# Performance work log

Measured on AMD Instinct MI355X. Metric: run time of the kernel, lower is better.

Reference implementation:

```python
import jax, jax.numpy as jnp
import numpy as np

N_NODES = 100_000
DEG = 16
N_EDGES = N_NODES * DEG
NODE_F = 128
EDGE_F = 16
HID = 64
B = 64
K = DEG


def setup_inputs() -> dict:
    key = jax.random.key(0)
    ks = jax.random.split(key, 12)
    # node i's outgoing edges are at ids i + k*N_NODES for k in [0, DEG)
    src = jnp.arange(N_EDGES, dtype=jnp.int32) % N_NODES
    dst = jax.random.randint(ks[0], (N_EDGES,), 0, N_NODES, dtype=jnp.int32)
    edge_index = jnp.stack([src, dst])
    current_nodes = jax.random.randint(ks[1], (B,), 0, N_NODES, dtype=jnp.int32)
    # reachable neighbors = destinations of the current node's real edges
    neighbor_nodes = dst[current_nodes[:, None] + jnp.arange(K, dtype=jnp.int32)[None, :] * N_NODES]
    x = jax.random.normal(ks[2], (N_NODES, NODE_F), jnp.float32)
    edge_attr = jax.random.normal(ks[3], (N_EDGES, EDGE_F), jnp.float32)
    return dict(
        x=x,
        edge_attr=edge_attr,
        conv1_W=jax.random.normal(ks[4], (NODE_F, HID), jnp.float32) * (NODE_F ** -0.5),
        conv1_b=jnp.zeros((HID,), jnp.float32),
        conv2_W=jax.random.normal(ks[5], (HID, HID), jnp.float32) * (HID ** -0.5),
        conv2_b=jnp.zeros((HID,), jnp.float32),
        mlp_W1=jax.random.normal(ks[6], (2 * HID + EDGE_F, 2 * HID), jnp.float32) * ((2 * HID + EDGE_F) ** -0.5),
        mlp_b1=jnp.zeros((2 * HID,), jnp.float32),
        mlp_W2=jax.random.normal(ks[7], (2 * HID, 1), jnp.float32) * ((2 * HID) ** -0.5),
        mlp_b2=jnp.zeros((1,), jnp.float32),
        edge_index=edge_index,
        current_nodes=current_nodes,
        neighbor_nodes=neighbor_nodes,
    )


def gcn_conv(x, edge_index, W, b):
    """PyG GCNConv: symmetric norm with self-loops, then linear + bias."""
    n = x.shape[0]
    loop = jnp.arange(n, dtype=edge_index.dtype)
    src = jnp.concatenate([edge_index[0], loop])  # messages flow src -> dst
    dst = jnp.concatenate([edge_index[1], loop])
    xw = x @ W                                    # [N, H]
    deg = jnp.zeros((n,), xw.dtype).at[dst].add(1.0)
    dinv = jnp.where(deg > 0, jax.lax.rsqrt(deg), 0.0)
    msg = (dinv[src] * dinv[dst])[:, None] * xw[src]      # [E+N, H]
    return jax.ops.segment_sum(msg, dst, num_segments=n) + b


def reference(x, edge_attr, conv1_W, conv1_b, conv2_W, conv2_b,
              mlp_W1, mlp_b1, mlp_W2, mlp_b2,
              edge_index, current_nodes, neighbor_nodes):
    n = x.shape[0]
    h = jax.nn.relu(gcn_conv(x, edge_index, conv1_W, conv1_b))
    h = jax.nn.relu(gcn_conv(h, edge_index, conv2_W, conv2_b))

    # First edge id matching each (current, neighbor) pair, replacing the
    # original O(E)-per-neighbor boolean-mask loop with a sorted-key lookup.
    keys = edge_index[0].astype(jnp.int64) * n + edge_index[1].astype(jnp.int64)
    order = jnp.argsort(keys, stable=True)        # stable -> leftmost == first edge id
    skeys = keys[order]
    query = current_nodes[:, None].astype(jnp.int64) * n + neighbor_nodes.astype(jnp.int64)
    pos = jnp.clip(jnp.searchsorted(skeys, query), 0, skeys.shape[0] - 1)
    valid = skeys[pos] == query                   # [B, K]
    eid = order[pos]
    ea = edge_attr[eid]                           # [B, K, F]

    b_, k_ = neighbor_nodes.shape
    h_cur = jnp.broadcast_to(h[current_nodes][:, None, :], (b_, k_, h.shape[1]))
    h_nbr = h[neighbor_nodes]
    m = jnp.concatenate([h_cur, h_nbr, ea], axis=-1)  # [B, K, 2H+F]
    q = (jax.nn.relu(m @ mlp_W1 + mlp_b1) @ mlp_W2 + mlp_b2)[..., 0]
    q = jnp.where(valid, q, 0.0)
    return q, valid
```

## Files before the change

kernel.cpp:

```cpp
#include <hip/hip_runtime.h>

#define N_NODES 100000
#define DEG 16
#define N_EDGES (N_NODES * DEG)
#define NODE_F 128
#define EDGE_F 16
#define HID 64
#define NQ 1024
#define NCHUNK (N_EDGES / 256)
#define XTILES ((N_NODES + 63) / 64)
#define NHIST 2048
#define BCAP 56
#define NDINV ((N_NODES + 255) / 256)
#define MAGIC 0x13579BDF

__device__ __forceinline__ int xcc_id() {
  int x;
  asm("s_getreg_b32 %0, hwreg(HW_REG_XCC_ID)" : "=s"(x));
  return x & 7;
}

__global__ void k_query_zero(const int* __restrict__ dst, const int* __restrict__ cur,
                             const int* __restrict__ nbr, int* __restrict__ n1,
                             int* __restrict__ n2, int* __restrict__ wcur,
                             int* __restrict__ eid_sel, float* __restrict__ out_valid,
                             int* __restrict__ degp) {
  if (blockIdx.x >= 4) {
    int4* d4 = (int4*)degp;
    const int n4 = 8 * N_NODES / 4;
    int i = (blockIdx.x - 4) * 256 + threadIdx.x;
    const int stride = (gridDim.x - 4) * 256;
    for (; i < n4; i += stride) d4[i] = make_int4(0, 0, 0, 0);
    return;
  }
  int i = blockIdx.x * 256 + threadIdx.x;
  if (i >= NQ) return;
  int b = i >> 4;
  int c = cur[b];
  int nb = nbr[i];
  int sel = -1;
  #pragma unroll
  for (int j = 0; j < DEG; ++j) {
    int e = c + j * N_NODES;
    if (sel < 0 && dst[e] == nb) sel = e;
  }
  eid_sel[i] = sel;
  out_valid[i] = (sel >= 0) ? 1.0f : 0.0f;
  n2[c] = MAGIC; n2[nb] = MAGIC;
  n1[c] = MAGIC; n1[nb] = MAGIC;
  wcur[c] = 0;   wcur[nb] = 0;
}

__global__ __launch_bounds__(256) void k_fusedA(
    const float* __restrict__ x, const float* __restrict__ Wg,
    float* __restrict__ xw, const int* __restrict__ dst,
    const int* __restrict__ n2, int* __restrict__ n1, int* __restrict__ wcur,
    int* __restrict__ degp) {
  __shared__ float xs[64 * 128];
  const int t = threadIdx.x;

  if (blockIdx.x < NHIST) {
    int* __restrict__ dp = degp + (size_t)xcc_id() * N_NODES;
    const int stride = NHIST * 256;
    for (int e = blockIdx.x * 256 + t; e < N_EDGES; e += stride) {
      int d = dst[e];
      __hip_atomic_fetch_add(&dp[d], 1, __ATOMIC_RELAXED,
                             __HIP_MEMORY_SCOPE_WORKGROUP);
      if (n2[d] == MAGIC) {
        int s = e % N_NODES;
        n1[s] = MAGIC;
        wcur[s] = 0;
      }
    }
    return;
  }

  const int lane = t & 63;
  const int w = __builtin_amdgcn_readfirstlane(t >> 6);
  const long base = (long)(blockIdx.x - NHIST) * 64;

  const float4* __restrict__ xv = (const float4*)x;
  #pragma unroll
  for (int p = 0; p < 8; ++p) {
    int f4 = p * 256 + t;
    int r = f4 >> 5;
    int c4 = f4 & 31;
    long gr = base + r;
    float4 v = (gr < N_NODES) ? xv[gr * 32 + c4]
                              : make_float4(0.f, 0.f, 0.f, 0.f);
    int rs = r & 31;
    float* xr = xs + r * 128;
    xr[((c4 << 2) + 0) ^ rs] = v.x;
    xr[((c4 << 2) + 1) ^ rs] = v.y;
    xr[((c4 << 2) + 2) ^ rs] = v.z;
    xr[((c4 << 2) + 3) ^ rs] = v.w;
  }
  __syncthreads();

  float acc[16];
  #pragma unroll
  for (int j = 0; j < 16; ++j) acc[j] = 0.f;
  const int ls = lane & 31;
  const float* __restrict__ xrow = xs + lane * 128;
  const float4* __restrict__ wp = (const float4*)(Wg + w * 16);
  #pragma unroll 4
  for (int k = 0; k < NODE_F; ++k) {
    float xk = xrow[k ^ ls];
    float4 w0 = wp[k * 16 + 0];
    float4 w1 = wp[k * 16 + 1];
    float4 w2 = wp[k * 16 + 2];
    float4 w3 = wp[k * 16 + 3];
    acc[ 0] = fmaf(xk, w0.x, acc[ 0]); acc[ 1] = fmaf(xk, w0.y, acc[ 1]);
    acc[ 2] = fmaf(xk, w0.z, acc[ 2]); acc[ 3] = fmaf(xk, w0.w, acc[ 3]);
    acc[ 4] = fmaf(xk, w1.x, acc[ 4]); acc[ 5] = fmaf(xk, w1.y, acc[ 5]);
    acc[ 6] = fmaf(xk, w1.z, acc[ 6]); acc[ 7] = fmaf(xk, w1.w, acc[ 7]);
    acc[ 8] = fmaf(xk, w2.x, acc[ 8]); acc[ 9] = fmaf(xk, w2.y, acc[ 9]);
    acc[10] = fmaf(xk, w2.z, acc[10]); acc[11] = fmaf(xk, w2.w, acc[11]);
    acc[12] = fmaf(xk, w3.x, acc[12]); acc[13] = fmaf(xk, w3.y, acc[13]);
    acc[14] = fmaf(xk, w3.z, acc[14]); acc[15] = fmaf(xk, w3.w, acc[15]);
  }
  long gr = base + lane;
  if (gr < N_NODES) {
    float4* __restrict__ op = (float4*)(xw + gr * HID + w * 16);
    op[0] = make_float4(acc[0], acc[1], acc[2], acc[3]);
    op[1] = make_float4(acc[4], acc[5], acc[6], acc[7]);
    op[2] = make_float4(acc[8], acc[9], acc[10], acc[11]);
    op[3] = make_float4(acc[12], acc[13], acc[14], acc[15]);
  }
}

__global__ void k_bucket_dinv(const int* __restrict__ dst, const int* __restrict__ n1,
                              int* __restrict__ wcur, int* __restrict__ bucket,
                              const int* __restrict__ degp, float* __restrict__ dinv) {
  if (blockIdx.x < NDINV) {
    int v = blockIdx.x * 256 + threadIdx.x;
    if (v < N_NODES) {
      int s = 1;
      #pragma unroll
      for (int p = 0; p < 8; ++p) s += degp[(size_t)p * N_NODES + v];
      dinv[v] = rsqrtf((float)s);
    }
    return;
  }
  int e = (blockIdx.x - NDINV) * 256 + threadIdx.x;
  int d = dst[e];
  if (n1[d] != MAGIC) return;
  int pos = atomicAdd(&wcur[d], 1);
  if (pos >= 0 && pos < BCAP)
    bucket[(size_t)d * BCAP + pos] = e % N_NODES;
}

__global__ __launch_bounds__(256) void k_gather_xw2(
    const int* __restrict__ bucket, const int* __restrict__ wcur,
    const int* __restrict__ n1, const float* __restrict__ dinv,
    const float* __restrict__ xw, const float* __restrict__ bias,
    const float* __restrict__ W2g, float* __restrict__ xw2) {
  const int t = threadIdx.x;
  const int lane = t & 63;
  const int v = blockIdx.x * 4 + (t >> 6);
  if (v >= N_NODES) return;
  if (n1[v] != MAGIC) return;
  int n = wcur[v];
  if (n > BCAP) n = BCAP;
  if (n < 0) n = 0;
  int   s_l = (lane < n) ? bucket[(size_t)v * BCAP + lane] : 0;
  float w_l = (lane < n) ? dinv[s_l] : 0.f;
  float acc = 0.f;
  int j = 0;
  for (; j + 3 < n; j += 4) {
    int s0 = __shfl(s_l, j);
    int s1 = __shfl(s_l, j + 1);
    int s2 = __shfl(s_l, j + 2);
    int s3 = __shfl(s_l, j + 3);
    float a0 = xw[(size_t)s0 * HID + lane];
    float a1 = xw[(size_t)s1 * HID + lane];
    float a2 = xw[(size_t)s2 * HID + lane];
    float a3 = xw[(size_t)s3 * HID + lane];
    acc = fmaf(__shfl(w_l, j), a0, acc);
    acc = fmaf(__shfl(w_l, j + 1), a1, acc);
    acc = fmaf(__shfl(w_l, j + 2), a2, acc);
    acc = fmaf(__shfl(w_l, j + 3), a3, acc);
  }
  for (; j < n; ++j)
    acc = fmaf(__shfl(w_l, j), xw[(size_t)__shfl(s_l, j) * HID + lane], acc);
  float dv = dinv[v];
  acc = fmaf(dv, xw[(size_t)v * HID + lane], acc);
  float h = fmaxf(fmaf(dv, acc, bias[lane]), 0.f);
  float a2s = 0.f;
  #pragma unroll
  for (int f = 0; f < HID; ++f)
    a2s = fmaf(__shfl(h, f), W2g[f * HID + lane], a2s);
  xw2[(size_t)v * HID + lane] = a2s;
}

__global__ __launch_bounds__(256) void k_gather(
    const int* __restrict__ bucket, const int* __restrict__ wcur,
    const int* __restrict__ flag, const float* __restrict__ dinv,
    const float* __restrict__ xw, const float* __restrict__ bias,
    float* __restrict__ hout) {
  const int t = threadIdx.x;
  const int lane = t & 63;
  const int v = blockIdx.x * 4 + (t >> 6);
  if (v >= N_NODES) return;
  if (flag[v] != MAGIC) return;
  int n = wcur[v];
  if (n > BCAP) n = BCAP;
  if (n < 0) n = 0;
  int   s_l = (lane < n) ? bucket[(size_t)v * BCAP + lane] : 0;
  float w_l = (lane < n) ? dinv[s_l] : 0.f;
  float acc = 0.f;
  int j = 0;
  for (; j + 3 < n; j += 4) {
    int s0 = __shfl(s_l, j);
    int s1 = __shfl(s_l, j + 1);
    int s2 = __shfl(s_l, j + 2);
    int s3 = __shfl(s_l, j + 3);
    float a0 = xw[(size_t)s0 * HID + lane];
    float a1 = xw[(size_t)s1 * HID + lane];
    float a2 = xw[(size_t)s2 * HID + lane];
    float a3 = xw[(size_t)s3 * HID + lane];
    acc = fmaf(__shfl(w_l, j), a0, acc);
    acc = fmaf(__shfl(w_l, j + 1), a1, acc);
    acc = fmaf(__shfl(w_l, j + 2), a2, acc);
    acc = fmaf(__shfl(w_l, j + 3), a3, acc);
  }
  for (; j < n; ++j)
    acc = fmaf(__shfl(w_l, j), xw[(size_t)__shfl(s_l, j) * HID + lane], acc);
  float dv = dinv[v];
  acc = fmaf(dv, xw[(size_t)v * HID + lane], acc);
  hout[(size_t)v * HID + lane] = fmaxf(fmaf(dv, acc, bias[lane]), 0.f);
}

__global__ void k_mlp(const float* __restrict__ h2, const float* __restrict__ ea,
                      const float* __restrict__ W1, const float* __restrict__ b1,
                      const float* __restrict__ W2, const float* __restrict__ b2,
                      const int* __restrict__ cur, const int* __restrict__ nbr,
                      const int* __restrict__ eid_sel, float* __restrict__ out) {
  __shared__ float m[2 * HID + EDGE_F];
  __shared__ float red[128];
  const int q = blockIdx.x;
  const int t = threadIdx.x;
  const int eid = eid_sel[q];
  if (eid < 0) {
    if (t == 0) out[q] = 0.0f;
    return;
  }
  const int b = q >> 4;
  const int c = cur[b];
  const int nb = nbr[q];
  if (t < HID)    m[t] = h2[(size_t)c * HID + t];
  else            m[t] = h2[(size_t)nb * HID + (t - HID)];
  if (t < EDGE_F) m[2 * HID + t] = ea[(size_t)eid * EDGE_F + t];
  __syncthreads();
  float h = b1[t];
  #pragma unroll
  for (int j = 0; j < 2 * HID + EDGE_F; ++j) h = fmaf(m[j], W1[j * 128 + t], h);
  h = fmaxf(h, 0.f) * W2[t];
  red[t] = h;
  __syncthreads();
  if (t < 64) {
    float v = red[t] + red[t + 64];
    #pragma unroll
    for (int o = 32; o > 0; o >>= 1) v += __shfl_down(v, o);
    if (t == 0) out[q] = v + b2[0];
  }
}

extern "C" void kernel_launch(void* const* d_in, const int* in_sizes, int n_in,
                              void* d_out, int out_size, void* d_ws, size_t ws_size,
                              hipStream_t stream) {
  const float* x    = (const float*)d_in[0];
  const float* ea   = (const float*)d_in[1];
  const float* c1W  = (const float*)d_in[2];
  const float* c1b  = (const float*)d_in[3];
  const float* c2W  = (const float*)d_in[4];
  const float* c2b  = (const float*)d_in[5];
  const float* mW1  = (const float*)d_in[6];
  const float* mb1  = (const float*)d_in[7];
  const float* mW2  = (const float*)d_in[8];
  const float* mb2  = (const float*)d_in[9];
  const int*   eidx = (const int*)d_in[10];
  const int*   cur  = (const int*)d_in[11];
  const int*   nbr  = (const int*)d_in[12];
  const int* edst = eidx + N_EDGES;
  float* out = (float*)d_out;

  char* p = (char*)d_ws;
  auto alloc = [&](size_t bytes) -> void* {
    void* r = (void*)p;
    p += (bytes + 255) & ~(size_t)255;
    return r;
  };
  int*   degp    = (int*)alloc((size_t)8 * N_NODES * 4);
  float* dinv    = (float*)alloc((size_t)N_NODES * 4);
  int*   n1      = (int*)alloc((size_t)N_NODES * 4);
  int*   n2      = (int*)alloc((size_t)N_NODES * 4);
  int*   wcur    = (int*)alloc((size_t)N_NODES * 4);
  int*   eid_sel = (int*)alloc((size_t)NQ * 4);
  int*   bucket  = (int*)alloc((size_t)N_NODES * BCAP * 4);
  float* xw1     = (float*)alloc((size_t)N_NODES * HID * 4);
  float* xw2     = (float*)alloc((size_t)N_NODES * HID * 4);
  float* h2      = xw1;

  k_query_zero<<<260, 256, 0, stream>>>(edst, cur, nbr, n1, n2, wcur, eid_sel,
                                        out + NQ, degp);
  k_fusedA<<<NHIST + XTILES, 256, 0, stream>>>(x, c1W, xw1, edst, n2, n1, wcur,
                                               degp);
  k_bucket_dinv<<<NDINV + NCHUNK, 256, 0, stream>>>(edst, n1, wcur, bucket, degp,
                                                    dinv);
  k_gather_xw2<<<(N_NODES + 3) / 4, 256, 0, stream>>>(bucket, wcur, n1, dinv, xw1,
                                                      c1b, c2W, xw2);
  k_gather<<<(N_NODES + 3) / 4, 256, 0, stream>>>(bucket, wcur, n2, dinv, xw2,
                                                  c2b, h2);
  k_mlp<<<NQ, 128, 0, stream>>>(h2, ea, mW1, mb1, mW2, mb2, cur, nbr, eid_sel, out);
}
```

Before: 356.0 us.

## Interleave histogram blocks among smaller 32-row GEMM tiles in fused kernel

```diff
diff --git a/kernel.cpp b/kernel.cpp
--- a/kernel.cpp
+++ b/kernel.cpp
@@ -8,8 +8,9 @@
 #define HID 64
 #define NQ 1024
 #define NCHUNK (N_EDGES / 256)
-#define XTILES ((N_NODES + 63) / 64)
 #define NHIST 2048
+#define XT32 (N_NODES / 32)
+#define TOTAL_A (NHIST + XT32)
 #define BCAP 56
 #define NDINV ((N_NODES + 255) / 256)
 #define MAGIC 0x13579BDF
@@ -56,13 +57,17 @@
     float* __restrict__ xw, const int* __restrict__ dst,
     const int* __restrict__ n2, int* __restrict__ n1, int* __restrict__ wcur,
     int* __restrict__ degp) {
-  __shared__ float xs[64 * 128];
+  __shared__ float xs[32 * 128];
   const int t = threadIdx.x;
-
-  if (blockIdx.x < NHIST) {
+  const int bid = blockIdx.x;
+
+  const int h0 = (int)(((long)bid * NHIST) / TOTAL_A);
+  const int h1b = (int)(((long)(bid + 1) * NHIST) / TOTAL_A);
+
+  if (h1b > h0) {
     int* __restrict__ dp = degp + (size_t)xcc_id() * N_NODES;
     const int stride = NHIST * 256;
-    for (int e = blockIdx.x * 256 + t; e < N_EDGES; e += stride) {
+    for (int e = h0 * 256 + t; e < N_EDGES; e += stride) {
       int d = dst[e];
       __hip_atomic_fetch_add(&dp[d], 1, __ATOMIC_RELAXED,
                              __HIP_MEMORY_SCOPE_WORKGROUP);
@@ -75,58 +80,44 @@
     return;
   }
 
-  const int lane = t & 63;
-  const int w = __builtin_amdgcn_readfirstlane(t >> 6);
-  const long base = (long)(blockIdx.x - NHIST) * 64;
+  const long base = (long)(bid - h0) * 32;
 
   const float4* __restrict__ xv = (const float4*)x;
   #pragma unroll
-  for (int p = 0; p < 8; ++p) {
+  for (int p = 0; p < 4; ++p) {
     int f4 = p * 256 + t;
     int r = f4 >> 5;
     int c4 = f4 & 31;
-    long gr = base + r;
-    float4 v = (gr < N_NODES) ? xv[gr * 32 + c4]
-                              : make_float4(0.f, 0.f, 0.f, 0.f);
-    int rs = r & 31;
+    float4 v = xv[(base + r) * 32 + c4];
     float* xr = xs + r * 128;
-    xr[((c4 << 2) + 0) ^ rs] = v.x;
-    xr[((c4 << 2) + 1) ^ rs] = v.y;
-    xr[((c4 << 2) + 2) ^ rs] = v.z;
-    xr[((c4 << 2) + 3) ^ rs] = v.w;
+    xr[((c4 << 2) + 0) ^ r] = v.x;
+    xr[((c4 << 2) + 1) ^ r] = v.y;
+    xr[((c4 << 2) + 2) ^ r] = v.z;
+    xr[((c4 << 2) + 3) ^ r] = v.w;
   }
   __syncthreads();
 
-  float acc[16];
-  #pragma unroll
-  for (int j = 0; j < 16; ++j) acc[j] = 0.f;
-  const int ls = lane & 31;
-  const float* __restrict__ xrow = xs + lane * 128;
-  const float4* __restrict__ wp = (const float4*)(Wg + w * 16);
+  float acc[8];
+  #pragma unroll
+  for (int j = 0; j < 8; ++j) acc[j] = 0.f;
+  const int r = t & 31;
+  const int cg = t >> 5;
+  const float* __restrict__ xrow = xs + r * 128;
+  const float4* __restrict__ wp = (const float4*)(Wg + cg * 8);
   #pragma unroll 4
   for (int k = 0; k < NODE_F; ++k) {
-    float xk = xrow[k ^ ls];
+    float xk = xrow[k ^ r];
     float4 w0 = wp[k * 16 + 0];
     float4 w1 = wp[k * 16 + 1];
-    float4 w2 = wp[k * 16 + 2];
-    float4 w3 = wp[k * 16 + 3];
-    acc[ 0] = fmaf(xk, w0.x, acc[ 0]); acc[ 1] = fmaf(xk, w0.y, acc[ 1]);
-    acc[ 2] = fmaf(xk, w0.z, acc[ 2]); acc[ 3] = fmaf(xk, w0.w, acc[ 3]);
-    acc[ 4] = fmaf(xk, w1.x, acc[ 4]); acc[ 5] = fmaf(xk, w1.y, acc[ 5]);
-    acc[ 6] = fmaf(xk, w1.z, acc[ 6]); acc[ 7] = fmaf(xk, w1.w, acc[ 7]);
-    acc[ 8] = fmaf(xk, w2.x, acc[ 8]); acc[ 9] = fmaf(xk, w2.y, acc[ 9]);
-    acc[10] = fmaf(xk, w2.z, acc[10]); acc[11] = fmaf(xk, w2.w, acc[11]);
-    acc[12] = fmaf(xk, w3.x, acc[12]); acc[13] = fmaf(xk, w3.y, acc[13]);
-    acc[14] = fmaf(xk, w3.z, acc[14]); acc[15] = fmaf(xk, w3.w, acc[15]);
-  }
-  long gr = base + lane;
-  if (gr < N_NODES) {
-    float4* __restrict__ op = (float4*)(xw + gr * HID + w * 16);
-    op[0] = make_float4(acc[0], acc[1], acc[2], acc[3]);
-    op[1] = make_float4(acc[4], acc[5], acc[6], acc[7]);
-    op[2] = make_float4(acc[8], acc[9], acc[10], acc[11]);
-    op[3] = make_float4(acc[12], acc[13], acc[14], acc[15]);
-  }
+    acc[0] = fmaf(xk, w0.x, acc[0]); acc[1] = fmaf(xk, w0.y, acc[1]);
+    acc[2] = fmaf(xk, w0.z, acc[2]); acc[3] = fmaf(xk, w0.w, acc[3]);
+    acc[4] = fmaf(xk, w1.x, acc[4]); acc[5] = fmaf(xk, w1.y, acc[5]);
+    acc[6] = fmaf(xk, w1.z, acc[6]); acc[7] = fmaf(xk, w1.w, acc[7]);
+  }
+  long gr = base + r;
+  float4* __restrict__ op = (float4*)(xw + gr * HID + cg * 8);
+  op[0] = make_float4(acc[0], acc[1], acc[2], acc[3]);
+  op[1] = make_float4(acc[4], acc[5], acc[6], acc[7]);
 }
 
 __global__ void k_bucket_dinv(const int* __restrict__ dst, const int* __restrict__ n1,
@@ -304,8 +295,7 @@
 
   k_query_zero<<<260, 256, 0, stream>>>(edst, cur, nbr, n1, n2, wcur, eid_sel,
                                         out + NQ, degp);
-  k_fusedA<<<NHIST + XTILES, 256, 0, stream>>>(x, c1W, xw1, edst, n2, n1, wcur,
-                                               degp);
+  k_fusedA<<<TOTAL_A, 256, 0, stream>>>(x, c1W, xw1, edst, n2, n1, wcur, degp);
   k_bucket_dinv<<<NDINV + NCHUNK, 256, 0, stream>>>(edst, n1, wcur, bucket, degp,
                                                     dinv);
   k_gather_xw2<<<(N_NODES + 3) / 4, 256, 0, stream>>>(bucket, wcur, n1, dinv, xw1,
```

After: 385.8 us. 8.4% more time.
